# Optimization experiments

Hardware: AMD Instinct MI355X
Metric: run time of the kernel (lower is better)

## Reference

```python
import jax
import jax.numpy as jnp
from jax import lax
import numpy as np

B, C, Hsp, Wsp = 16, 256, 64, 64
E, HID = 4, 128          # num_experts, expert_hidden
RH = 128                 # router_hidden
TOP_K = 1
EPS = 1e-9


def setup_inputs() -> dict:
    key = jax.random.key(0)
    ks = jax.random.split(key, 8)
    s = lambda *shape: 1.0 / np.sqrt(shape[-1])
    x = jax.random.normal(ks[0], (B, C, Hsp, Wsp), dtype=jnp.float32)
    # router: Linear(C->RH), Linear(RH->E)
    Wr1 = jax.random.normal(ks[1], (RH, C), dtype=jnp.float32) * s(RH, C)
    br1 = jnp.zeros((RH,), dtype=jnp.float32)
    Wr2 = jax.random.normal(ks[2], (E, RH), dtype=jnp.float32) * s(E, RH)
    br2 = jnp.zeros((E,), dtype=jnp.float32)
    # experts (stacked over E): 1x1 C->HID, 3x3 HID->HID, 1x1 HID->C, all bias-free
    W1 = jax.random.normal(ks[3], (E, HID, C), dtype=jnp.float32) * s(E, HID, C)
    W2 = jax.random.normal(ks[4], (E, HID, HID, 3, 3), dtype=jnp.float32) * (1.0 / np.sqrt(HID * 9))
    W3 = jax.random.normal(ks[5], (E, C, HID), dtype=jnp.float32) * s(E, C, HID)
    return {"x": x, "Wr1": Wr1, "br1": br1, "Wr2": Wr2, "br2": br2,
            "W1": W1, "W2": W2, "W3": W3}


def reference(x, Wr1, br1, Wr2, br2, W1, W2, W3):
    b = x.shape[0]
    # --- router on globally pooled features ---
    pooled = x.mean(axis=(2, 3))                      # [B, C]
    h = jax.nn.relu(pooled @ Wr1.T + br1)             # [B, RH]
    logits = h @ Wr2.T + br2                          # [B, E]
    probs = jax.nn.softmax(logits, axis=1)
    # top-k masking + renormalize (top_k < num_experts)
    vals, idx = lax.top_k(probs, TOP_K)               # [B, k]
    mask = jnp.zeros_like(probs).at[jnp.arange(b)[:, None], idx].set(vals)
    probs = mask / (mask.sum(axis=1, keepdims=True) + EPS)
    # --- run all experts (as in original) ---
    # 1x1 conv C->HID, per expert:  [B, E, HID, H, W]
    y1 = jax.nn.relu(jnp.einsum('bcij,ehc->behij', x, W1))
    # 3x3 grouped conv (one group per expert), HID->HID
    y1m = y1.reshape(b, E * HID, Hsp, Wsp)
    y2 = lax.conv_general_dilated(
        y1m, W2.reshape(E * HID, HID, 3, 3),
        window_strides=(1, 1), padding='SAME',
        feature_group_count=E,
        dimension_numbers=('NCHW', 'OIHW', 'NCHW'))
    y2 = jax.nn.relu(y2).reshape(b, E, HID, Hsp, Wsp)
    # 1x1 conv HID->C fused with routed weighted sum over experts + residual
    out = jnp.einsum('begij,ecg,be->bcij', y2, W3, probs) + x
    return out
```

## Files before the change

### kernel.cpp

```cpp
#include <hip/hip_runtime.h>

typedef unsigned short ushort_t;
typedef unsigned int uint32;
typedef __attribute__((ext_vector_type(8))) short s16x8;
typedef __attribute__((ext_vector_type(4))) float f32x4;

#define BB   16
#define CC   256
#define NPX  4096
#define EE   4
#define HID  128
#define RHH  128
#define PW   66
#define PPX  (66*66)

__device__ __forceinline__ ushort_t f2bf(float f) {
  uint32 x = __float_as_uint(f);
  x += 0x7fffu + ((x >> 16) & 1u);
  return (ushort_t)(x >> 16);
}
__device__ __forceinline__ void g2l16(const void* g, void* l) {
  __builtin_amdgcn_global_load_lds((const __attribute__((address_space(1))) uint32*)g,
                                   (__attribute__((address_space(3))) uint32*)l, 16, 0, 0);
}

__global__ __launch_bounds__(256)
void k_prep(const float* __restrict__ x, float* __restrict__ pooled,
            const float* __restrict__ W1f, const float* __restrict__ W3f,
            const float* __restrict__ W2f, ushort_t* __restrict__ W1b,
            ushort_t* __restrict__ W3b, ushort_t* __restrict__ W2r,
            ushort_t* __restrict__ y1Tp) {
  int bid = blockIdx.x, t = threadIdx.x;
  if (bid < 4096) {
    int c = bid & 255, b = bid >> 8;
    const float* xg = x + ((size_t)b * CC + c) * NPX;
    float s = 0.f;
#pragma unroll
    for (int k = 0; k < 4; ++k) {
      float4 v = *(const float4*)(xg + (size_t)(k * 256 + t) * 4);
      s += v.x + v.y + v.z + v.w;
    }
#pragma unroll
    for (int o = 32; o >= 1; o >>= 1) s += __shfl_down(s, o, 64);
    __shared__ float wsum[4];
    if ((t & 63) == 0) wsum[t >> 6] = s;
    __syncthreads();
    if (t == 0) pooled[(size_t)b * CC + c] = wsum[0] + wsum[1] + wsum[2] + wsum[3];
  } else if (bid < 4352) {
    int i4 = ((bid - 4096) * 256 + t) * 4;
    const float* src; ushort_t* dst; int off;
    if (i4 < EE * HID * CC) { src = W1f; dst = W1b; off = i4; }
    else { src = W3f; dst = W3b; off = i4 - EE * HID * CC; }
    float4 v = *(const float4*)(src + off);
    ushort4 o;
    o.x = f2bf(v.x); o.y = f2bf(v.y); o.z = f2bf(v.z); o.w = f2bf(v.w);
    *(ushort4*)(dst + off) = o;
  } else if (bid < 4480) {
    int idx = (bid - 4352) * 256 + t;
    int e = idx >> 13;
    int o = (idx >> 6) & 127;
    int ip = (idx & 63) * 2;
    const float* s0 = W2f + ((size_t)((e * 128 + o) * 128) + ip) * 9;
    float v0[9], v1[9];
#pragma unroll
    for (int tp = 0; tp < 9; ++tp) { v0[tp] = s0[tp]; v1[tp] = s0[9 + tp]; }
#pragma unroll
    for (int tp = 0; tp < 9; ++tp) {
      uint32 w = (uint32)f2bf(v0[tp]) | ((uint32)f2bf(v1[tp]) << 16);
      *(uint32*)&W2r[(((size_t)(e * 9 + tp) * 128 + o) * 128) + ip] = w;
    }
  } else {
    int p = (bid - 4480) * 8 + (t >> 5);
    int b = p / 260, i = p % 260;
    int row, col;
    if (i < 66)       { row = 0;       col = i; }
    else if (i < 132) { row = 65;      col = i - 66; }
    else if (i < 196) { row = i - 131; col = 0; }
    else              { row = i - 195; col = 65; }
    uint2* dst = (uint2*)(y1Tp + (((size_t)b * PPX + row * PW + col) * HID) + (t & 31) * 4);
    *dst = make_uint2(0u, 0u);
  }
}

__global__ __launch_bounds__(128)
void k_router(const float* __restrict__ pooled, const float* __restrict__ Wr1,
              const float* __restrict__ br1, const float* __restrict__ Wr2,
              const float* __restrict__ br2, int* __restrict__ eidx,
              float* __restrict__ gatew) {
  int b = blockIdx.x, t = threadIdx.x;
  __shared__ float spool[CC];
  __shared__ float hb[RHH];
  __shared__ float lg[EE];
  for (int cc = t; cc < CC; cc += 128) spool[cc] = pooled[(size_t)b * CC + cc];
  __syncthreads();
  float s0 = 0.f;
  const float* wr = Wr1 + t * CC;
  for (int c = 0; c < CC; ++c) s0 += spool[c] * wr[c];
  float a = br1[t] + s0 * (1.0f / NPX);
  hb[t] = a > 0.f ? a : 0.f;
  __syncthreads();
  if (t < EE) {
    float s = br2[t];
    const float* w2 = Wr2 + t * RHH;
    for (int r = 0; r < RHH; ++r) s += hb[r] * w2[r];
    lg[t] = s;
  }
  __syncthreads();
  if (t == 0) {
    float m = lg[0]; int mi = 0;
    for (int e = 1; e < EE; ++e) if (lg[e] > m) { m = lg[e]; mi = e; }
    float den = 0.f;
    for (int e = 0; e < EE; ++e) den += expf(lg[e] - m);
    float v = 1.0f / den;
    eidx[b] = mi;
    gatew[b] = v / (v + 1e-9f);
  }
}

#define STAGE64B(dstB, srcB_expr)                                         \
  {                                                                       \
    _Pragma("unroll")                                                     \
    for (int s_ = 0; s_ < 4; ++s_) {                                      \
      int ch_ = wave * 4 + s_;                                            \
      int r = ch_ * 8 + (lane >> 3);                                      \
      int kc = ((lane & 7) ^ (lane >> 3)) * 8;                            \
      g2l16(srcB_expr, &dstB[ch_ * 512]);                                 \
    }                                                                     \
  }

#define STAGEW(dst, wsrc, k0v)                                            \
  {                                                                       \
    _Pragma("unroll")                                                     \
    for (int s_ = 0; s_ < 4; ++s_) {                                      \
      int ch_ = wave * 4 + s_;                                            \
      int r_ = ch_ * 8 + (lane >> 3);                                     \
      int kc_ = ((lane & 7) ^ (lane >> 3)) * 8;                           \
      g2l16(wsrc + (size_t)r_ * HID + (k0v) + kc_, &dst[ch_ * 512]);      \
    }                                                                     \
  }

#define MFMA64(At_, Bt_, ACC_)                                            \
  _Pragma("unroll")                                                       \
  for (int kh = 0; kh < 2; ++kh) {                                        \
    s16x8 af[4], bfr[4];                                                  \
    int cidx = ((kh * 4 + (lane >> 4)) ^ (lane & 7)) * 8;                 \
    _Pragma("unroll")                                                     \
    for (int i = 0; i < 4; ++i)                                           \
      af[i] = *(const s16x8*)&At_[(wm + i * 16 + (lane & 15)) * 64 + cidx]; \
    _Pragma("unroll")                                                     \
    for (int j = 0; j < 4; ++j)                                           \
      bfr[j] = *(const s16x8*)&Bt_[(wn + j * 16 + (lane & 15)) * 64 + cidx]; \
    _Pragma("unroll")                                                     \
    for (int i = 0; i < 4; ++i)                                           \
      _Pragma("unroll")                                                   \
      for (int j = 0; j < 4; ++j)                                         \
        ACC_[i][j] = __builtin_amdgcn_mfma_f32_16x16x32_bf16(af[i], bfr[j], ACC_[i][j], 0, 0, 0); \
  }

#define MFMA64H(Hs_, dyv, dxv, Bt_, ACC_)                                 \
  {                                                                       \
    int hbase = ((wm >> 6) + 1 + (dyv)) * 66 + (lane & 15) + 1 + (dxv);   \
    _Pragma("unroll")                                                     \
    for (int kh = 0; kh < 2; ++kh) {                                      \
      s16x8 af[4], bfr[4];                                                \
      int clog = kh * 4 + (lane >> 4);                                    \
      int aoff = (clog ^ (hbase & 7)) << 3;                               \
      int cidx = (clog ^ (lane & 7)) << 3;                                \
      _Pragma("unroll")                                                   \
      for (int i = 0; i < 4; ++i)                                         \
        af[i] = *(const s16x8*)&Hs_[(hbase + i * 16) * 64 + aoff];        \
      _Pragma("unroll")                                                   \
      for (int j = 0; j < 4; ++j)                                         \
        bfr[j] = *(const s16x8*)&Bt_[(wn + j * 16 + (lane & 15)) * 64 + cidx]; \
      _Pragma("unroll")                                                   \
      for (int i = 0; i < 4; ++i)                                         \
        _Pragma("unroll")                                                 \
        for (int j = 0; j < 4; ++j)                                       \
          ACC_[i][j] = __builtin_amdgcn_mfma_f32_16x16x32_bf16(af[i], bfr[j], ACC_[i][j], 0, 0, 0); \
    }                                                                     \
  }

__global__ __launch_bounds__(256)
void k_conv1(const float* __restrict__ x, const ushort_t* __restrict__ W1b,
             const int* __restrict__ eidx, ushort_t* __restrict__ y1Tp) {
  int mt = blockIdx.x, b = blockIdx.y;
  int e = eidx[b];
  int t = threadIdx.x, wave = t >> 6, lane = t & 63;
  int wm = (wave & 1) * 64, wn = (wave >> 1) * 64;
  __shared__ ushort_t smem[128 * 128];
  ushort_t* At = smem;
  ushort_t* Bt = smem + 128 * 64;
  f32x4 acc[4][4] = {};
  const float* xg = x + (size_t)b * CC * NPX + mt * 128;
  const ushort_t* w1 = W1b + (size_t)e * HID * CC;

  int cp = t >> 3;
  int kk = cp * 2;
  int pxb = (t & 7) * 4;

  for (int ks = 0; ks < 4; ++ks) {
    int k0 = ks * 64;
    __syncthreads();
    STAGE64B(Bt, w1 + (size_t)r * CC + k0 + kc);
    {
      const float* r0 = xg + (size_t)(k0 + kk) * NPX;
      const float* r1 = r0 + NPX;
#pragma unroll
      for (int i = 0; i < 4; ++i) {
        int p = pxb + i * 32;
        float4 va = *(const float4*)(r0 + p);
        float4 vb = *(const float4*)(r1 + p);
#pragma unroll
        for (int q = 0; q < 4; ++q) {
          int m = p + q;
          uint32 v = (uint32)f2bf(((const float*)&va)[q]) |
                     ((uint32)f2bf(((const float*)&vb)[q]) << 16);
          int us = m * 64 + (((kk >> 3) ^ (m & 7)) << 3) + (kk & 7);
          *(uint32*)&At[us] = v;
        }
      }
    }
    __syncthreads();
    MFMA64(At, Bt, acc);
  }
  __syncthreads();
#pragma unroll
  for (int i = 0; i < 4; ++i)
#pragma unroll
    for (int j = 0; j < 4; ++j)
#pragma unroll
      for (int r = 0; r < 4; ++r) {
        int m = wm + i * 16 + (lane >> 4) * 4 + r;
        int n = wn + j * 16 + (lane & 15);
        float v = acc[i][j][r];
        smem[m * 128 + (((n >> 3) ^ (m & 7)) << 3) + (n & 7)] = f2bf(v > 0.f ? v : 0.f);
      }
  __syncthreads();
  ushort_t* yb = y1Tp + (size_t)b * PPX * HID;
#pragma unroll
  for (int it = 0; it < 8; ++it) {
    int idx = it * 256 + t;
    int row = idx >> 4, ch = idx & 15;
    int prow = mt * 2 + (row >> 6) + 1, pcol = (row & 63) + 1;
    uint4 v = *(const uint4*)&smem[row * 128 + ((ch ^ (row & 7)) << 3)];
    *(uint4*)(yb + ((size_t)prow * PW + pcol) * HID + ch * 8) = v;
  }
}

__global__ __launch_bounds__(256, 2)
void k_conv23(const ushort_t* __restrict__ y1Tp, const ushort_t* __restrict__ W2r,
              const ushort_t* __restrict__ W3b, const float* __restrict__ x,
              const int* __restrict__ eidx, const float* __restrict__ gatew,
              float* __restrict__ out) {
  int mt = blockIdx.x, b = blockIdx.y;
  int e = eidx[b];
  float gw = gatew[b];
  int t = threadIdx.x, wave = t >> 6, lane = t & 63;
  int wm = (wave & 1) * 64, wn = (wave >> 1) * 64;
  __shared__ ushort_t Hs[4 * 66 * 64];
  __shared__ ushort_t Wb0[128 * 64];
  __shared__ ushort_t Wb1[128 * 64];
  const ushort_t* yb = y1Tp + (size_t)b * PPX * HID;
  const ushort_t* w2e = W2r + (size_t)e * 9 * HID * HID;
  asm volatile("" :: "v"(gw), "s"(e));

  f32x4 acc[4][4] = {};
  for (int ks = 0; ks < 2; ++ks) {
    int k0 = ks * 64;
    __syncthreads();
#pragma unroll
    for (int it = 0; it < 9; ++it) {
      if (it < 8 || wave == 0) {
        int q = it * 256 + t;
        int p = q >> 3, slot = q & 7;
        g2l16(yb + ((size_t)(mt * 132 + p)) * HID + k0 + ((slot ^ (p & 7)) << 3),
              &Hs[(it * 256 + wave * 64) * 8]);
      }
    }
    STAGEW(Wb0, w2e + 0 * HID * HID, k0);
    __syncthreads();
#pragma unroll
    for (int tap = 0; tap < 9; ++tap) {
      ushort_t* cur = (tap & 1) ? Wb1 : Wb0;
      ushort_t* nxt = (tap & 1) ? Wb0 : Wb1;
      if (tap < 8) {
        STAGEW(nxt, w2e + (tap + 1) * HID * HID, k0);
        asm volatile("s_waitcnt vmcnt(4)" ::: "memory");
      } else {
        asm volatile("s_waitcnt vmcnt(0)" ::: "memory");
      }
      __builtin_amdgcn_s_barrier();
      MFMA64H(Hs, tap / 3 - 1, tap % 3 - 1, cur, acc);
      __builtin_amdgcn_s_barrier();
    }
  }
  ushort_t (*y2s)[128 * 64] = (ushort_t (*)[128 * 64])Hs;
#pragma unroll
  for (int i = 0; i < 4; ++i)
#pragma unroll
    for (int j = 0; j < 4; ++j)
#pragma unroll
      for (int r = 0; r < 4; ++r) {
        int m = wm + i * 16 + (lane >> 4) * 4 + r;
        int n = wn + j * 16 + (lane & 15);
        float v = acc[i][j][r];
        ushort_t bv = f2bf(v > 0.f ? v : 0.f);
        int nn = n & 63;
        ushort_t* buf = (n < 64) ? y2s[0] : y2s[1];
        buf[m * 64 + ((nn >> 3) ^ (m & 7)) * 8 + (nn & 7)] = bv;
      }
  f32x4 acc3[2][4][4] = {};
  const ushort_t* w3 = W3b + (size_t)e * CC * HID;
#pragma unroll
  for (int h = 0; h < 2; ++h) {
#pragma unroll
    for (int ks = 0; ks < 2; ++ks) {
      ushort_t* bt = (ks == 0) ? Wb0 : Wb1;
      STAGEW(bt, w3 + (size_t)h * 128 * HID, ks * 64);
      __syncthreads();
      MFMA64(y2s[ks], bt, acc3[h]);
    }
  }
  float* Tf = (float*)Hs;
  for (int h = 0; h < 2; ++h) {
    for (int jj = 0; jj < 4; ++jj) {
      __syncthreads();
      if ((wn >> 6) == (jj >> 1)) {
        int j0 = (jj & 1) * 2;
#pragma unroll
        for (int jd = 0; jd < 2; ++jd) {
          int cl = jd * 16 + (lane & 15);
#pragma unroll
          for (int i = 0; i < 4; ++i) {
            int pb = wm + i * 16 + (lane >> 4) * 4;
            *(f32x4*)&Tf[cl * 132 + pb] = acc3[h][i][j0 + jd];
          }
        }
      }
      __syncthreads();
#pragma unroll
      for (int it = 0; it < 4; ++it) {
        int idx = it * 256 + t;
        int crow = idx >> 5;
        int p4 = (idx & 31) * 4;
        int c = h * 128 + jj * 32 + crow;
        int px = mt * 128 + p4;
        size_t base = ((size_t)b * CC + c) * NPX + px;
        f32x4 vv = *(const f32x4*)&Tf[crow * 132 + p4];
        f32x4 xa = *(const f32x4*)(x + base);
        vv = gw * vv + xa;
        __builtin_nontemporal_store(vv, (f32x4*)(out + base));
      }
    }
  }
}

extern "C" void kernel_launch(void* const* d_in, const int* in_sizes, int n_in,
                              void* d_out, int out_size, void* d_ws, size_t ws_size,
                              hipStream_t stream) {
  const float* x   = (const float*)d_in[0];
  const float* Wr1 = (const float*)d_in[1];
  const float* br1 = (const float*)d_in[2];
  const float* Wr2 = (const float*)d_in[3];
  const float* br2 = (const float*)d_in[4];
  const float* W1  = (const float*)d_in[5];
  const float* W2  = (const float*)d_in[6];
  const float* W3  = (const float*)d_in[7];
  float* out = (float*)d_out;

  char* ws = (char*)d_ws;
  int*      eidx   = (int*)ws;
  float*    gatew  = (float*)(ws + 64);
  float*    pooled = (float*)(ws + 256);
  ushort_t* W1b    = (ushort_t*)(ws + 16640);
  ushort_t* W3b    = (ushort_t*)(ws + 278784);
  ushort_t* W2r    = (ushort_t*)(ws + 540928);
  ushort_t* y1Tp   = (ushort_t*)(ws + 1720576);

  k_prep  <<<5000, 256, 0, stream>>>(x, pooled, W1, W3, W2, W1b, W3b, W2r, y1Tp);
  k_router<<<16, 128, 0, stream>>>(pooled, Wr1, br1, Wr2, br2, eidx, gatew);
  k_conv1 <<<dim3(32, 16), 256, 0, stream>>>(x, W1b, eidx, y1Tp);
  k_conv23<<<dim3(32, 16), 256, 0, stream>>>(y1Tp, W2r, W3b, x, eidx, gatew, out);
}
```

Baseline: 184.7 us.

## Inline router into conv kernels and pipeline weight/halo/residual loads

Removes the separate router kernel launch. Each conv block now recomputes the router inline from the pooled features, using a transposed Wr1 that k_prep writes for coalesced reads. In k_conv23 the 3x3 tap loop is software-pipelined across both K halves and into the W3 stage, and the second halo load moves to after the first half. W3 staging is double-buffered, and x residual loads are prefetched one step ahead of the epilogue stores. MFMA sections get raised wave priority. This trades redundant per-block router work and more barriers for one fewer launch and better load/compute overlap.

```diff
diff --git a/kernel.cpp b/kernel.cpp
--- a/kernel.cpp
+++ b/kernel.cpp
@@ -24,11 +24,16 @@
                                    (__attribute__((address_space(3))) uint32*)l, 16, 0, 0);
 }
 
+#define LGKM0  asm volatile("s_waitcnt lgkmcnt(0)" ::: "memory")
+#define SBAR   __builtin_amdgcn_s_barrier()
+#define SCHED0 __builtin_amdgcn_sched_barrier(0)
+
 __global__ __launch_bounds__(256)
 void k_prep(const float* __restrict__ x, float* __restrict__ pooled,
             const float* __restrict__ W1f, const float* __restrict__ W3f,
-            const float* __restrict__ W2f, ushort_t* __restrict__ W1b,
-            ushort_t* __restrict__ W3b, ushort_t* __restrict__ W2r,
+            const float* __restrict__ W2f, const float* __restrict__ Wr1,
+            ushort_t* __restrict__ W1b, ushort_t* __restrict__ W3b,
+            ushort_t* __restrict__ W2r, float* __restrict__ Wr1T,
             ushort_t* __restrict__ y1Tp) {
   int bid = blockIdx.x, t = threadIdx.x;
   if (bid < 4096) {
@@ -69,8 +74,16 @@
       uint32 w = (uint32)f2bf(v0[tp]) | ((uint32)f2bf(v1[tp]) << 16);
       *(uint32*)&W2r[(((size_t)(e * 9 + tp) * 128 + o) * 128) + ip] = w;
     }
+  } else if (bid < 4512) {
+    int i4 = ((bid - 4480) * 256 + t) * 4;
+    int rh = i4 >> 8, c = i4 & 255;
+    float4 v = *(const float4*)(Wr1 + i4);
+    Wr1T[(size_t)(c + 0) * RHH + rh] = v.x;
+    Wr1T[(size_t)(c + 1) * RHH + rh] = v.y;
+    Wr1T[(size_t)(c + 2) * RHH + rh] = v.z;
+    Wr1T[(size_t)(c + 3) * RHH + rh] = v.w;
   } else {
-    int p = (bid - 4480) * 8 + (t >> 5);
+    int p = (bid - 4512) * 8 + (t >> 5);
     int b = p / 260, i = p % 260;
     int row, col;
     if (i < 66)       { row = 0;       col = i; }
@@ -79,41 +92,6 @@
     else              { row = i - 195; col = 65; }
     uint2* dst = (uint2*)(y1Tp + (((size_t)b * PPX + row * PW + col) * HID) + (t & 31) * 4);
     *dst = make_uint2(0u, 0u);
-  }
-}
-
-__global__ __launch_bounds__(128)
-void k_router(const float* __restrict__ pooled, const float* __restrict__ Wr1,
-              const float* __restrict__ br1, const float* __restrict__ Wr2,
-              const float* __restrict__ br2, int* __restrict__ eidx,
-              float* __restrict__ gatew) {
-  int b = blockIdx.x, t = threadIdx.x;
-  __shared__ float spool[CC];
-  __shared__ float hb[RHH];
-  __shared__ float lg[EE];
-  for (int cc = t; cc < CC; cc += 128) spool[cc] = pooled[(size_t)b * CC + cc];
-  __syncthreads();
-  float s0 = 0.f;
-  const float* wr = Wr1 + t * CC;
-  for (int c = 0; c < CC; ++c) s0 += spool[c] * wr[c];
-  float a = br1[t] + s0 * (1.0f / NPX);
-  hb[t] = a > 0.f ? a : 0.f;
-  __syncthreads();
-  if (t < EE) {
-    float s = br2[t];
-    const float* w2 = Wr2 + t * RHH;
-    for (int r = 0; r < RHH; ++r) s += hb[r] * w2[r];
-    lg[t] = s;
-  }
-  __syncthreads();
-  if (t == 0) {
-    float m = lg[0]; int mi = 0;
-    for (int e = 1; e < EE; ++e) if (lg[e] > m) { m = lg[e]; mi = e; }
-    float den = 0.f;
-    for (int e = 0; e < EE; ++e) den += expf(lg[e] - m);
-    float v = 1.0f / den;
-    eidx[b] = mi;
-    gatew[b] = v / (v + 1e-9f);
   }
 }
 
@@ -180,16 +158,57 @@
     }                                                                     \
   }
 
+__device__ __forceinline__ void router_inline(
+    const float* __restrict__ pooled, const float* __restrict__ Wr1T,
+    const float* __restrict__ br1, const float* __restrict__ Wr2,
+    const float* __restrict__ br2, float* scratch, int b, int t,
+    int* e_out, float* gw_out) {
+  float* spool = scratch;
+  float* hbp   = spool + 256;
+  float* lgp   = hbp + 128;
+  float* gwp   = lgp + 4;
+  int*   eip   = (int*)(gwp + 1);
+  if (t < 64) ((float4*)spool)[t] = ((const float4*)(pooled + (size_t)b * CC))[t];
+  LGKM0; SBAR; SCHED0;
+  if (t < RHH) {
+    float aa = 0.f;
+    for (int c = 0; c < CC; ++c) aa += spool[c] * Wr1T[(size_t)c * RHH + t];
+    float av = br1[t] + aa * (1.0f / NPX);
+    hbp[t] = av > 0.f ? av : 0.f;
+  }
+  LGKM0; SBAR; SCHED0;
+  if (t < EE) {
+    float sv = br2[t];
+    const float* w2 = Wr2 + t * RHH;
+    for (int r = 0; r < RHH; ++r) sv += hbp[r] * w2[r];
+    lgp[t] = sv;
+  }
+  LGKM0; SBAR; SCHED0;
+  if (t == 0) {
+    float m = lgp[0]; int mi = 0;
+    for (int ee = 1; ee < EE; ++ee) if (lgp[ee] > m) { m = lgp[ee]; mi = ee; }
+    float den = 0.f;
+    for (int ee = 0; ee < EE; ++ee) den += expf(lgp[ee] - m);
+    float v = 1.0f / den;
+    *eip = mi; *gwp = v / (v + 1e-9f);
+  }
+  LGKM0; SBAR; SCHED0;
+  *e_out = *eip; *gw_out = *gwp;
+}
+
 __global__ __launch_bounds__(256)
 void k_conv1(const float* __restrict__ x, const ushort_t* __restrict__ W1b,
-             const int* __restrict__ eidx, ushort_t* __restrict__ y1Tp) {
+             const float* __restrict__ pooled, const float* __restrict__ Wr1T,
+             const float* __restrict__ br1, const float* __restrict__ Wr2,
+             const float* __restrict__ br2, ushort_t* __restrict__ y1Tp) {
   int mt = blockIdx.x, b = blockIdx.y;
-  int e = eidx[b];
   int t = threadIdx.x, wave = t >> 6, lane = t & 63;
   int wm = (wave & 1) * 64, wn = (wave >> 1) * 64;
   __shared__ ushort_t smem[128 * 128];
   ushort_t* At = smem;
   ushort_t* Bt = smem + 128 * 64;
+  int e; float gw;
+  router_inline(pooled, Wr1T, br1, Wr2, br2, (float*)smem, b, t, &e, &gw);
   f32x4 acc[4][4] = {};
   const float* xg = x + (size_t)b * CC * NPX + mt * 128;
   const ushort_t* w1 = W1b + (size_t)e * HID * CC;
@@ -250,24 +269,18 @@
 __global__ __launch_bounds__(256, 2)
 void k_conv23(const ushort_t* __restrict__ y1Tp, const ushort_t* __restrict__ W2r,
               const ushort_t* __restrict__ W3b, const float* __restrict__ x,
-              const int* __restrict__ eidx, const float* __restrict__ gatew,
-              float* __restrict__ out) {
+              const float* __restrict__ pooled, const float* __restrict__ Wr1T,
+              const float* __restrict__ br1, const float* __restrict__ Wr2,
+              const float* __restrict__ br2, float* __restrict__ out) {
   int mt = blockIdx.x, b = blockIdx.y;
-  int e = eidx[b];
-  float gw = gatew[b];
   int t = threadIdx.x, wave = t >> 6, lane = t & 63;
   int wm = (wave & 1) * 64, wn = (wave >> 1) * 64;
   __shared__ ushort_t Hs[4 * 66 * 64];
   __shared__ ushort_t Wb0[128 * 64];
   __shared__ ushort_t Wb1[128 * 64];
   const ushort_t* yb = y1Tp + (size_t)b * PPX * HID;
-  const ushort_t* w2e = W2r + (size_t)e * 9 * HID * HID;
-  asm volatile("" :: "v"(gw), "s"(e));
-
-  f32x4 acc[4][4] = {};
-  for (int ks = 0; ks < 2; ++ks) {
-    int k0 = ks * 64;
-    __syncthreads();
+
+  auto halo_stage = [&](int k0) {
 #pragma unroll
     for (int it = 0; it < 9; ++it) {
       if (it < 8 || wave == 0) {
@@ -277,22 +290,35 @@
               &Hs[(it * 256 + wave * 64) * 8]);
       }
     }
-    STAGEW(Wb0, w2e + 0 * HID * HID, k0);
-    __syncthreads();
+  };
+
+  halo_stage(0);
+  int e; float gw;
+  router_inline(pooled, Wr1T, br1, Wr2, br2, (float*)Wb1, b, t, &e, &gw);
+  const ushort_t* w2e = W2r + (size_t)e * 9 * HID * HID;
+  const ushort_t* w3  = W3b + (size_t)e * CC * HID;
+  STAGEW(Wb0, w2e, 0);
+  __syncthreads();
+
+  f32x4 acc[4][4] = {};
+#pragma unroll
+  for (int ks = 0; ks < 2; ++ks) {
 #pragma unroll
     for (int tap = 0; tap < 9; ++tap) {
-      ushort_t* cur = (tap & 1) ? Wb1 : Wb0;
-      ushort_t* nxt = (tap & 1) ? Wb0 : Wb1;
-      if (tap < 8) {
-        STAGEW(nxt, w2e + (tap + 1) * HID * HID, k0);
-        asm volatile("s_waitcnt vmcnt(4)" ::: "memory");
-      } else {
-        asm volatile("s_waitcnt vmcnt(0)" ::: "memory");
-      }
-      __builtin_amdgcn_s_barrier();
+      int par = (tap + ks * 9) & 1;
+      ushort_t* cur = par ? Wb1 : Wb0;
+      ushort_t* nxt = par ? Wb0 : Wb1;
+      if (tap < 8)       { STAGEW(nxt, w2e + (size_t)(tap + 1) * HID * HID, ks * 64); }
+      else if (ks == 0)  { STAGEW(nxt, w2e, 64); }
+      else               { STAGEW(nxt, w3, 0); }
+      asm volatile("s_waitcnt vmcnt(4)" ::: "memory");
+      SBAR; SCHED0;
+      __builtin_amdgcn_s_setprio(1);
       MFMA64H(Hs, tap / 3 - 1, tap % 3 - 1, cur, acc);
-      __builtin_amdgcn_s_barrier();
-    }
+      __builtin_amdgcn_s_setprio(0);
+      SBAR;
+    }
+    if (ks == 0) halo_stage(64);
   }
   ushort_t (*y2s)[128 * 64] = (ushort_t (*)[128 * 64])Hs;
 #pragma unroll
@@ -310,48 +336,68 @@
         buf[m * 64 + ((nn >> 3) ^ (m & 7)) * 8 + (nn & 7)] = bv;
       }
   f32x4 acc3[2][4][4] = {};
-  const ushort_t* w3 = W3b + (size_t)e * CC * HID;
-#pragma unroll
-  for (int h = 0; h < 2; ++h) {
-#pragma unroll
-    for (int ks = 0; ks < 2; ++ks) {
-      ushort_t* bt = (ks == 0) ? Wb0 : Wb1;
-      STAGEW(bt, w3 + (size_t)h * 128 * HID, ks * 64);
-      __syncthreads();
-      MFMA64(y2s[ks], bt, acc3[h]);
-    }
+#pragma unroll
+  for (int s = 0; s < 4; ++s) {
+    ushort_t* cur = (s & 1) ? Wb1 : Wb0;
+    ushort_t* nxt = (s & 1) ? Wb0 : Wb1;
+    if (s < 3) {
+      int s1 = s + 1;
+      STAGEW(nxt, w3 + (size_t)((s1 >> 1) * 128) * HID, (s1 & 1) * 64);
+      asm volatile("s_waitcnt vmcnt(4)" ::: "memory");
+    } else {
+      asm volatile("s_waitcnt vmcnt(0)" ::: "memory");
+    }
+    if (s == 0) LGKM0;
+    SBAR; SCHED0;
+    __builtin_amdgcn_s_setprio(1);
+    MFMA64(y2s[s & 1], cur, acc3[s >> 1]);
+    __builtin_amdgcn_s_setprio(0);
+    SBAR;
   }
   float* Tf = (float*)Hs;
-  for (int h = 0; h < 2; ++h) {
-    for (int jj = 0; jj < 4; ++jj) {
-      __syncthreads();
-      if ((wn >> 6) == (jj >> 1)) {
-        int j0 = (jj & 1) * 2;
-#pragma unroll
-        for (int jd = 0; jd < 2; ++jd) {
-          int cl = jd * 16 + (lane & 15);
-#pragma unroll
-          for (int i = 0; i < 4; ++i) {
-            int pb = wm + i * 16 + (lane >> 4) * 4;
-            *(f32x4*)&Tf[cl * 132 + pb] = acc3[h][i][j0 + jd];
-          }
+  const float* xb = x + (size_t)b * CC * NPX + mt * 128;
+  f32x4 xpre[4];
+#pragma unroll
+  for (int it = 0; it < 4; ++it) {
+    int idx = it * 256 + t, crow = idx >> 5, p4 = (idx & 31) * 4;
+    xpre[it] = *(const f32x4*)(xb + (size_t)crow * NPX + p4);
+  }
+#pragma unroll
+  for (int s = 0; s < 8; ++s) {
+    int h = s >> 2, jj = s & 3;
+    if ((wn >> 6) == (jj >> 1)) {
+      int j0 = (jj & 1) * 2;
+#pragma unroll
+      for (int jd = 0; jd < 2; ++jd) {
+        int cl = jd * 16 + (lane & 15);
+#pragma unroll
+        for (int i = 0; i < 4; ++i) {
+          int pb = wm + i * 16 + (lane >> 4) * 4;
+          *(f32x4*)&Tf[cl * 132 + pb] = acc3[h][i][j0 + jd];
         }
       }
-      __syncthreads();
+    }
+    LGKM0; SBAR; SCHED0;
+    f32x4 xc[4];
+#pragma unroll
+    for (int it = 0; it < 4; ++it) xc[it] = xpre[it];
+    if (s < 7) {
+      int s1 = s + 1, h1 = s1 >> 2, jj1 = s1 & 3;
 #pragma unroll
       for (int it = 0; it < 4; ++it) {
-        int idx = it * 256 + t;
-        int crow = idx >> 5;
-        int p4 = (idx & 31) * 4;
-        int c = h * 128 + jj * 32 + crow;
-        int px = mt * 128 + p4;
-        size_t base = ((size_t)b * CC + c) * NPX + px;
-        f32x4 vv = *(const f32x4*)&Tf[crow * 132 + p4];
-        f32x4 xa = *(const f32x4*)(x + base);
-        vv = gw * vv + xa;
-        __builtin_nontemporal_store(vv, (f32x4*)(out + base));
-      }
-    }
+        int idx = it * 256 + t, crow = idx >> 5, p4 = (idx & 31) * 4;
+        xpre[it] = *(const f32x4*)(xb + (size_t)(h1 * 128 + jj1 * 32 + crow) * NPX + p4);
+      }
+    }
+#pragma unroll
+    for (int it = 0; it < 4; ++it) {
+      int idx = it * 256 + t, crow = idx >> 5, p4 = (idx & 31) * 4;
+      int c = h * 128 + jj * 32 + crow;
+      f32x4 vv = *(const f32x4*)&Tf[crow * 132 + p4];
+      vv = gw * vv + xc[it];
+      __builtin_nontemporal_store(vv, (f32x4*)(out + ((size_t)b * CC + c) * NPX + mt * 128 + p4));
+    }
+    SBAR;
   }
 }
 
@@ -369,16 +415,14 @@
   float* out = (float*)d_out;
 
   char* ws = (char*)d_ws;
-  int*      eidx   = (int*)ws;
-  float*    gatew  = (float*)(ws + 64);
   float*    pooled = (float*)(ws + 256);
   ushort_t* W1b    = (ushort_t*)(ws + 16640);
   ushort_t* W3b    = (ushort_t*)(ws + 278784);
   ushort_t* W2r    = (ushort_t*)(ws + 540928);
-  ushort_t* y1Tp   = (ushort_t*)(ws + 1720576);
-
-  k_prep  <<<5000, 256, 0, stream>>>(x, pooled, W1, W3, W2, W1b, W3b, W2r, y1Tp);
-  k_router<<<16, 128, 0, stream>>>(pooled, Wr1, br1, Wr2, br2, eidx, gatew);
-  k_conv1 <<<dim3(32, 16), 256, 0, stream>>>(x, W1b, eidx, y1Tp);
-  k_conv23<<<dim3(32, 16), 256, 0, stream>>>(y1Tp, W2r, W3b, x, eidx, gatew, out);
-}
+  float*    Wr1T   = (float*)(ws + 1720576);
+  ushort_t* y1Tp   = (ushort_t*)(ws + 1851648);
+
+  k_prep  <<<5032, 256, 0, stream>>>(x, pooled, W1, W3, W2, Wr1, W1b, W3b, W2r, Wr1T, y1Tp);
+  k_conv1 <<<dim3(32, 16), 256, 0, stream>>>(x, W1b, pooled, Wr1T, br1, Wr2, br2, y1Tp);
+  k_conv23<<<dim3(32, 16), 256, 0, stream>>>(y1Tp, W2r, W3b, x, pooled, Wr1T, br1, Wr2, br2, out);
+}
```

New measurement: 203.6 us. +10.2%, slower.

## Fuse expert 1x1 conv into the 3x3/1x1 conv kernel with halo recompute

Applied to the files above, without the earlier changes.

Removes the separate conv1 kernel and its padded bf16 y1 intermediate in global memory. Each block now computes its own y1 tile, including a one-row halo above and below, directly from x into shared memory, zero-fills the left and right padding columns, and then runs the 3x3 and final 1x1 convs. This saves a kernel launch and the global write and read of y1, and the prep kernel no longer zeroes the padding. In exchange, the halo rows mean each block does about twice the conv1 MFMA work and reads more x, and the per-block dependency chain gets longer.

```diff
diff --git a/kernel.cpp b/kernel.cpp
--- a/kernel.cpp
+++ b/kernel.cpp
@@ -11,8 +11,6 @@
 #define EE   4
 #define HID  128
 #define RHH  128
-#define PW   66
-#define PPX  (66*66)
 
 __device__ __forceinline__ ushort_t f2bf(float f) {
   uint32 x = __float_as_uint(f);
@@ -28,8 +26,7 @@
 void k_prep(const float* __restrict__ x, float* __restrict__ pooled,
             const float* __restrict__ W1f, const float* __restrict__ W3f,
             const float* __restrict__ W2f, ushort_t* __restrict__ W1b,
-            ushort_t* __restrict__ W3b, ushort_t* __restrict__ W2r,
-            ushort_t* __restrict__ y1Tp) {
+            ushort_t* __restrict__ W3b, ushort_t* __restrict__ W2r) {
   int bid = blockIdx.x, t = threadIdx.x;
   if (bid < 4096) {
     int c = bid & 255, b = bid >> 8;
@@ -55,7 +52,7 @@
     ushort4 o;
     o.x = f2bf(v.x); o.y = f2bf(v.y); o.z = f2bf(v.z); o.w = f2bf(v.w);
     *(ushort4*)(dst + off) = o;
-  } else if (bid < 4480) {
+  } else {
     int idx = (bid - 4352) * 256 + t;
     int e = idx >> 13;
     int o = (idx >> 6) & 127;
@@ -69,16 +66,6 @@
       uint32 w = (uint32)f2bf(v0[tp]) | ((uint32)f2bf(v1[tp]) << 16);
       *(uint32*)&W2r[(((size_t)(e * 9 + tp) * 128 + o) * 128) + ip] = w;
     }
-  } else {
-    int p = (bid - 4480) * 8 + (t >> 5);
-    int b = p / 260, i = p % 260;
-    int row, col;
-    if (i < 66)       { row = 0;       col = i; }
-    else if (i < 132) { row = 65;      col = i - 66; }
-    else if (i < 196) { row = i - 131; col = 0; }
-    else              { row = i - 195; col = 65; }
-    uint2* dst = (uint2*)(y1Tp + (((size_t)b * PPX + row * PW + col) * HID) + (t & 31) * 4);
-    *dst = make_uint2(0u, 0u);
   }
 }
 
@@ -117,17 +104,6 @@
   }
 }
 
-#define STAGE64B(dstB, srcB_expr)                                         \
-  {                                                                       \
-    _Pragma("unroll")                                                     \
-    for (int s_ = 0; s_ < 4; ++s_) {                                      \
-      int ch_ = wave * 4 + s_;                                            \
-      int r = ch_ * 8 + (lane >> 3);                                      \
-      int kc = ((lane & 7) ^ (lane >> 3)) * 8;                            \
-      g2l16(srcB_expr, &dstB[ch_ * 512]);                                 \
-    }                                                                     \
-  }
-
 #define STAGEW(dst, wsrc, k0v)                                            \
   {                                                                       \
     _Pragma("unroll")                                                     \
@@ -180,111 +156,109 @@
     }                                                                     \
   }
 
-__global__ __launch_bounds__(256)
-void k_conv1(const float* __restrict__ x, const ushort_t* __restrict__ W1b,
-             const int* __restrict__ eidx, ushort_t* __restrict__ y1Tp) {
-  int mt = blockIdx.x, b = blockIdx.y;
-  int e = eidx[b];
-  int t = threadIdx.x, wave = t >> 6, lane = t & 63;
-  int wm = (wave & 1) * 64, wn = (wave >> 1) * 64;
-  __shared__ ushort_t smem[128 * 128];
-  ushort_t* At = smem;
-  ushort_t* Bt = smem + 128 * 64;
-  f32x4 acc[4][4] = {};
-  const float* xg = x + (size_t)b * CC * NPX + mt * 128;
-  const ushort_t* w1 = W1b + (size_t)e * HID * CC;
-
-  int cp = t >> 3;
-  int kk = cp * 2;
-  int pxb = (t & 7) * 4;
-
-  for (int ks = 0; ks < 4; ++ks) {
-    int k0 = ks * 64;
-    __syncthreads();
-    STAGE64B(Bt, w1 + (size_t)r * CC + k0 + kc);
-    {
-      const float* r0 = xg + (size_t)(k0 + kk) * NPX;
-      const float* r1 = r0 + NPX;
-#pragma unroll
-      for (int i = 0; i < 4; ++i) {
-        int p = pxb + i * 32;
-        float4 va = *(const float4*)(r0 + p);
-        float4 vb = *(const float4*)(r1 + p);
-#pragma unroll
-        for (int q = 0; q < 4; ++q) {
-          int m = p + q;
-          uint32 v = (uint32)f2bf(((const float*)&va)[q]) |
-                     ((uint32)f2bf(((const float*)&vb)[q]) << 16);
-          int us = m * 64 + (((kk >> 3) ^ (m & 7)) << 3) + (kk & 7);
-          *(uint32*)&At[us] = v;
-        }
-      }
-    }
-    __syncthreads();
-    MFMA64(At, Bt, acc);
-  }
-  __syncthreads();
-#pragma unroll
-  for (int i = 0; i < 4; ++i)
-#pragma unroll
-    for (int j = 0; j < 4; ++j)
-#pragma unroll
-      for (int r = 0; r < 4; ++r) {
-        int m = wm + i * 16 + (lane >> 4) * 4 + r;
-        int n = wn + j * 16 + (lane & 15);
-        float v = acc[i][j][r];
-        smem[m * 128 + (((n >> 3) ^ (m & 7)) << 3) + (n & 7)] = f2bf(v > 0.f ? v : 0.f);
-      }
-  __syncthreads();
-  ushort_t* yb = y1Tp + (size_t)b * PPX * HID;
-#pragma unroll
-  for (int it = 0; it < 8; ++it) {
-    int idx = it * 256 + t;
-    int row = idx >> 4, ch = idx & 15;
-    int prow = mt * 2 + (row >> 6) + 1, pcol = (row & 63) + 1;
-    uint4 v = *(const uint4*)&smem[row * 128 + ((ch ^ (row & 7)) << 3)];
-    *(uint4*)(yb + ((size_t)prow * PW + pcol) * HID + ch * 8) = v;
-  }
-}
-
 __global__ __launch_bounds__(256, 2)
-void k_conv23(const ushort_t* __restrict__ y1Tp, const ushort_t* __restrict__ W2r,
-              const ushort_t* __restrict__ W3b, const float* __restrict__ x,
-              const int* __restrict__ eidx, const float* __restrict__ gatew,
-              float* __restrict__ out) {
+void k_fused(const float* __restrict__ x, const ushort_t* __restrict__ W1b,
+             const ushort_t* __restrict__ W2r, const ushort_t* __restrict__ W3b,
+             const int* __restrict__ eidx, const float* __restrict__ gatew,
+             float* __restrict__ out) {
   int mt = blockIdx.x, b = blockIdx.y;
   int e = eidx[b];
   float gw = gatew[b];
   int t = threadIdx.x, wave = t >> 6, lane = t & 63;
   int wm = (wave & 1) * 64, wn = (wave >> 1) * 64;
   __shared__ ushort_t Hs[4 * 66 * 64];
-  __shared__ ushort_t Wb0[128 * 64];
-  __shared__ ushort_t Wb1[128 * 64];
-  const ushort_t* yb = y1Tp + (size_t)b * PPX * HID;
+  __shared__ ushort_t WbA[2 * 128 * 64];
+  ushort_t* Wb0 = WbA;
+  ushort_t* Wb1 = WbA + 128 * 64;
   const ushort_t* w2e = W2r + (size_t)e * 9 * HID * HID;
-  asm volatile("" :: "v"(gw), "s"(e));
+  const float* xg = x + (size_t)b * CC * NPX;
+  int px0 = mt * 128 - 64;
+  int cp = t >> 3, kk = cp * 2, pxb = (t & 7) * 4;
 
   f32x4 acc[4][4] = {};
-  for (int ks = 0; ks < 2; ++ks) {
-    int k0 = ks * 64;
+#pragma unroll 1
+  for (int kh = 0; kh < 2; ++kh) {
+    int k0 = kh * 64;
+    f32x4 acc1[4][4] = {};
+    const ushort_t* w1h = W1b + ((size_t)e * HID + k0) * CC;
+#pragma unroll 1
+    for (int cc = 0; cc < 4; ++cc) {
+      int c0 = cc * 64;
+      __syncthreads();
+      {
+#pragma unroll
+        for (int s_ = 0; s_ < 2; ++s_) {
+          int ch2 = wave * 128 + s_ * 64 + lane;
+          int r_ = ch2 >> 3, slot = ch2 & 7;
+          g2l16(w1h + (size_t)r_ * CC + c0 + ((slot ^ (r_ & 7)) << 3),
+                &Hs[(wave * 128 + s_ * 64) * 8]);
+        }
+      }
+      {
+        const float* r0 = xg + (size_t)(c0 + kk) * NPX + px0;
+        const float* r1 = r0 + NPX;
+#pragma unroll
+        for (int i = 0; i < 8; ++i) {
+          int p = pxb + i * 32;
+          int rp = px0 + p;
+          float4 va, vb;
+          if (rp >= 0 && rp < NPX) { va = *(const float4*)(r0 + p); vb = *(const float4*)(r1 + p); }
+          else { va = make_float4(0.f, 0.f, 0.f, 0.f); vb = va; }
+#pragma unroll
+          for (int q = 0; q < 4; ++q) {
+            int m = p + q;
+            uint32 v = (uint32)f2bf(((const float*)&va)[q]) |
+                       ((uint32)f2bf(((const float*)&vb)[q]) << 16);
+            int us = m * 64 + (((kk >> 3) ^ (m & 7)) << 3) + (kk & 7);
+            *(uint32*)&WbA[us] = v;
+          }
+        }
+      }
+      __syncthreads();
+#pragma unroll
+      for (int khk = 0; khk < 2; ++khk) {
+        s16x8 af[4], bfr[4];
+        int clog = khk * 4 + (lane >> 4);
+        int cidx = (clog ^ (lane & 7)) * 8;
+#pragma unroll
+        for (int i = 0; i < 4; ++i)
+          af[i] = *(const s16x8*)&WbA[(wave * 64 + i * 16 + (lane & 15)) * 64 + cidx];
+#pragma unroll
+        for (int j = 0; j < 4; ++j)
+          bfr[j] = *(const s16x8*)&Hs[(j * 16 + (lane & 15)) * 64 + cidx];
+#pragma unroll
+        for (int i = 0; i < 4; ++i)
+#pragma unroll
+          for (int j = 0; j < 4; ++j)
+            acc1[i][j] = __builtin_amdgcn_mfma_f32_16x16x32_bf16(af[i], bfr[j], acc1[i][j], 0, 0, 0);
+      }
+    }
     __syncthreads();
-#pragma unroll
-    for (int it = 0; it < 9; ++it) {
-      if (it < 8 || wave == 0) {
-        int q = it * 256 + t;
-        int p = q >> 3, slot = q & 7;
-        g2l16(yb + ((size_t)(mt * 132 + p)) * HID + k0 + ((slot ^ (p & 7)) << 3),
-              &Hs[(it * 256 + wave * 64) * 8]);
-      }
-    }
-    STAGEW(Wb0, w2e + 0 * HID * HID, k0);
+    STAGEW(Wb0, w2e, k0);
+#pragma unroll
+    for (int i = 0; i < 4; ++i)
+#pragma unroll
+      for (int j = 0; j < 4; ++j)
+#pragma unroll
+        for (int r = 0; r < 4; ++r) {
+          int m = wave * 64 + i * 16 + (lane >> 4) * 4 + r;
+          int h = j * 16 + (lane & 15);
+          int pix = (m >> 6) * 66 + (m & 63) + 1;
+          float v = acc1[i][j][r];
+          Hs[pix * 64 + (((h >> 3) ^ (pix & 7)) << 3) + (h & 7)] = f2bf(v > 0.f ? v : 0.f);
+        }
+    {
+      int row8 = t >> 5;
+      int pix = (row8 >> 1) * 66 + (row8 & 1) * 65;
+      ((uint32*)&Hs[pix * 64])[t & 31] = 0u;
+    }
     __syncthreads();
 #pragma unroll
     for (int tap = 0; tap < 9; ++tap) {
       ushort_t* cur = (tap & 1) ? Wb1 : Wb0;
       ushort_t* nxt = (tap & 1) ? Wb0 : Wb1;
       if (tap < 8) {
-        STAGEW(nxt, w2e + (tap + 1) * HID * HID, k0);
+        STAGEW(nxt, w2e + (size_t)(tap + 1) * HID * HID, k0);
         asm volatile("s_waitcnt vmcnt(4)" ::: "memory");
       } else {
         asm volatile("s_waitcnt vmcnt(0)" ::: "memory");
@@ -294,6 +268,7 @@
       __builtin_amdgcn_s_barrier();
     }
   }
+  __syncthreads();
   ushort_t (*y2s)[128 * 64] = (ushort_t (*)[128 * 64])Hs;
 #pragma unroll
   for (int i = 0; i < 4; ++i)
@@ -316,7 +291,7 @@
 #pragma unroll
     for (int ks = 0; ks < 2; ++ks) {
       ushort_t* bt = (ks == 0) ? Wb0 : Wb1;
-      STAGEW(bt, w3 + (size_t)h * 128 * HID, ks * 64);
+      STAGEW(bt, w3 + (size_t)(h * 128) * HID, ks * 64);
       __syncthreads();
       MFMA64(y2s[ks], bt, acc3[h]);
     }
@@ -375,10 +350,8 @@
   ushort_t* W1b    = (ushort_t*)(ws + 16640);
   ushort_t* W3b    = (ushort_t*)(ws + 278784);
   ushort_t* W2r    = (ushort_t*)(ws + 540928);
-  ushort_t* y1Tp   = (ushort_t*)(ws + 1720576);
-
-  k_prep  <<<5000, 256, 0, stream>>>(x, pooled, W1, W3, W2, W1b, W3b, W2r, y1Tp);
+
+  k_prep  <<<4480, 256, 0, stream>>>(x, pooled, W1, W3, W2, W1b, W3b, W2r);
   k_router<<<16, 128, 0, stream>>>(pooled, Wr1, br1, Wr2, br2, eidx, gatew);
-  k_conv1 <<<dim3(32, 16), 256, 0, stream>>>(x, W1b, eidx, y1Tp);
-  k_conv23<<<dim3(32, 16), 256, 0, stream>>>(y1Tp, W2r, W3b, x, eidx, gatew, out);
-}
+  k_fused <<<dim3(32, 16), 256, 0, stream>>>(x, W1b, W2r, W3b, eidx, gatew, out);
+}
```

Result: slower. 238.9 us (+29.3%).

## Fuse router into pooling kernel via last-block atomic counter; prefetch x in conv1

Applied to the files above, without the earlier changes.

Removes the separate router kernel launch. Each batch's 256 pooling blocks bump an atomic counter, and the last block to finish computes the router MLP, softmax and top-1 in place. This needs a memset of the counters before each run. Separately, conv1 now register-prefetches the next K-slice of x during the MFMA, hiding global load latency at the cost of more registers. A barrier is also added before the conv3 stage.

```diff
diff --git a/kernel.cpp b/kernel.cpp
--- a/kernel.cpp
+++ b/kernel.cpp
@@ -26,9 +26,14 @@
 
 __global__ __launch_bounds__(256)
 void k_prep(const float* __restrict__ x, float* __restrict__ pooled,
+            int* __restrict__ cnt,
             const float* __restrict__ W1f, const float* __restrict__ W3f,
-            const float* __restrict__ W2f, ushort_t* __restrict__ W1b,
-            ushort_t* __restrict__ W3b, ushort_t* __restrict__ W2r,
+            const float* __restrict__ W2f, const float* __restrict__ Wr1,
+            const float* __restrict__ br1, const float* __restrict__ Wr2,
+            const float* __restrict__ br2,
+            ushort_t* __restrict__ W1b, ushort_t* __restrict__ W3b,
+            ushort_t* __restrict__ W2r,
+            int* __restrict__ eidx, float* __restrict__ gatew,
             ushort_t* __restrict__ y1Tp) {
   int bid = blockIdx.x, t = threadIdx.x;
   if (bid < 4096) {
@@ -43,9 +48,62 @@
 #pragma unroll
     for (int o = 32; o >= 1; o >>= 1) s += __shfl_down(s, o, 64);
     __shared__ float wsum[4];
+    __shared__ int lastf;
     if ((t & 63) == 0) wsum[t >> 6] = s;
     __syncthreads();
-    if (t == 0) pooled[(size_t)b * CC + c] = wsum[0] + wsum[1] + wsum[2] + wsum[3];
+    if (t == 0) {
+      float tot = wsum[0] + wsum[1] + wsum[2] + wsum[3];
+      __hip_atomic_store(&pooled[(size_t)b * CC + c], tot,
+                         __ATOMIC_RELEASE, __HIP_MEMORY_SCOPE_AGENT);
+      int old = __hip_atomic_fetch_add(&cnt[b], 1,
+                                       __ATOMIC_ACQ_REL, __HIP_MEMORY_SCOPE_AGENT);
+      lastf = (old == 255) ? 1 : 0;
+    }
+    __syncthreads();
+    if (lastf) {
+      __shared__ float spool[CC];
+      __shared__ float ha[256];
+      __shared__ float hbuf[RHH];
+      __shared__ float lg2[8];
+      spool[t] = __hip_atomic_load(&pooled[(size_t)b * CC + t],
+                                   __ATOMIC_ACQUIRE, __HIP_MEMORY_SCOPE_AGENT);
+      __syncthreads();
+      {
+        int rh = t & 127, hf = t >> 7;
+        const float* wr = Wr1 + (size_t)rh * CC + hf * 128;
+        const float* sp = spool + hf * 128;
+        float a = 0.f;
+        for (int c2 = 0; c2 < 128; ++c2) a += sp[c2] * wr[c2];
+        ha[hf * 128 + rh] = a;
+      }
+      __syncthreads();
+      if (t < RHH) {
+        float av = br1[t] + (ha[t] + ha[128 + t]) * (1.0f / NPX);
+        hbuf[t] = av > 0.f ? av : 0.f;
+      }
+      __syncthreads();
+      if (t < 8) {
+        int e4 = t & 3, hf = t >> 2;
+        const float* w2 = Wr2 + (size_t)e4 * RHH + hf * 64;
+        const float* hh = hbuf + hf * 64;
+        float sv = 0.f;
+        for (int r = 0; r < 64; ++r) sv += hh[r] * w2[r];
+        lg2[t] = sv;
+      }
+      __syncthreads();
+      if (t == 0) {
+        float lgv[4];
+#pragma unroll
+        for (int ee = 0; ee < 4; ++ee) lgv[ee] = br2[ee] + lg2[ee] + lg2[4 + ee];
+        float m = lgv[0]; int mi = 0;
+        for (int ee = 1; ee < 4; ++ee) if (lgv[ee] > m) { m = lgv[ee]; mi = ee; }
+        float den = 0.f;
+        for (int ee = 0; ee < 4; ++ee) den += expf(lgv[ee] - m);
+        float v = 1.0f / den;
+        eidx[b] = mi;
+        gatew[b] = v / (v + 1e-9f);
+      }
+    }
   } else if (bid < 4352) {
     int i4 = ((bid - 4096) * 256 + t) * 4;
     const float* src; ushort_t* dst; int off;
@@ -79,41 +137,6 @@
     else              { row = i - 195; col = 65; }
     uint2* dst = (uint2*)(y1Tp + (((size_t)b * PPX + row * PW + col) * HID) + (t & 31) * 4);
     *dst = make_uint2(0u, 0u);
-  }
-}
-
-__global__ __launch_bounds__(128)
-void k_router(const float* __restrict__ pooled, const float* __restrict__ Wr1,
-              const float* __restrict__ br1, const float* __restrict__ Wr2,
-              const float* __restrict__ br2, int* __restrict__ eidx,
-              float* __restrict__ gatew) {
-  int b = blockIdx.x, t = threadIdx.x;
-  __shared__ float spool[CC];
-  __shared__ float hb[RHH];
-  __shared__ float lg[EE];
-  for (int cc = t; cc < CC; cc += 128) spool[cc] = pooled[(size_t)b * CC + cc];
-  __syncthreads();
-  float s0 = 0.f;
-  const float* wr = Wr1 + t * CC;
-  for (int c = 0; c < CC; ++c) s0 += spool[c] * wr[c];
-  float a = br1[t] + s0 * (1.0f / NPX);
-  hb[t] = a > 0.f ? a : 0.f;
-  __syncthreads();
-  if (t < EE) {
-    float s = br2[t];
-    const float* w2 = Wr2 + t * RHH;
-    for (int r = 0; r < RHH; ++r) s += hb[r] * w2[r];
-    lg[t] = s;
-  }
-  __syncthreads();
-  if (t == 0) {
-    float m = lg[0]; int mi = 0;
-    for (int e = 1; e < EE; ++e) if (lg[e] > m) { m = lg[e]; mi = e; }
-    float den = 0.f;
-    for (int e = 0; e < EE; ++e) den += expf(lg[e] - m);
-    float v = 1.0f / den;
-    eidx[b] = mi;
-    gatew[b] = v / (v + 1e-9f);
   }
 }
 
@@ -198,29 +221,44 @@
   int kk = cp * 2;
   int pxb = (t & 7) * 4;
 
+  float4 va[4], vb[4];
+  {
+    const float* r0 = xg + (size_t)kk * NPX;
+    const float* r1 = r0 + NPX;
+#pragma unroll
+    for (int i = 0; i < 4; ++i) {
+      va[i] = *(const float4*)(r0 + pxb + i * 32);
+      vb[i] = *(const float4*)(r1 + pxb + i * 32);
+    }
+  }
   for (int ks = 0; ks < 4; ++ks) {
     int k0 = ks * 64;
     __syncthreads();
     STAGE64B(Bt, w1 + (size_t)r * CC + k0 + kc);
     {
-      const float* r0 = xg + (size_t)(k0 + kk) * NPX;
-      const float* r1 = r0 + NPX;
 #pragma unroll
       for (int i = 0; i < 4; ++i) {
         int p = pxb + i * 32;
-        float4 va = *(const float4*)(r0 + p);
-        float4 vb = *(const float4*)(r1 + p);
 #pragma unroll
         for (int q = 0; q < 4; ++q) {
           int m = p + q;
-          uint32 v = (uint32)f2bf(((const float*)&va)[q]) |
-                     ((uint32)f2bf(((const float*)&vb)[q]) << 16);
+          uint32 v = (uint32)f2bf(((const float*)&va[i])[q]) |
+                     ((uint32)f2bf(((const float*)&vb[i])[q]) << 16);
           int us = m * 64 + (((kk >> 3) ^ (m & 7)) << 3) + (kk & 7);
           *(uint32*)&At[us] = v;
         }
       }
     }
     __syncthreads();
+    if (ks < 3) {
+      const float* r0 = xg + (size_t)(k0 + 64 + kk) * NPX;
+      const float* r1 = r0 + NPX;
+#pragma unroll
+      for (int i = 0; i < 4; ++i) {
+        va[i] = *(const float4*)(r0 + pxb + i * 32);
+        vb[i] = *(const float4*)(r1 + pxb + i * 32);
+      }
+    }
     MFMA64(At, Bt, acc);
   }
   __syncthreads();
@@ -277,14 +315,14 @@
               &Hs[(it * 256 + wave * 64) * 8]);
       }
     }
-    STAGEW(Wb0, w2e + 0 * HID * HID, k0);
+    STAGEW(Wb0, w2e, k0);
     __syncthreads();
 #pragma unroll
     for (int tap = 0; tap < 9; ++tap) {
       ushort_t* cur = (tap & 1) ? Wb1 : Wb0;
       ushort_t* nxt = (tap & 1) ? Wb0 : Wb1;
       if (tap < 8) {
-        STAGEW(nxt, w2e + (tap + 1) * HID * HID, k0);
+        STAGEW(nxt, w2e + (size_t)(tap + 1) * HID * HID, k0);
         asm volatile("s_waitcnt vmcnt(4)" ::: "memory");
       } else {
         asm volatile("s_waitcnt vmcnt(0)" ::: "memory");
@@ -309,6 +347,7 @@
         ushort_t* buf = (n < 64) ? y2s[0] : y2s[1];
         buf[m * 64 + ((nn >> 3) ^ (m & 7)) * 8 + (nn & 7)] = bv;
       }
+  __syncthreads();
   f32x4 acc3[2][4][4] = {};
   const ushort_t* w3 = W3b + (size_t)e * CC * HID;
 #pragma unroll
@@ -316,7 +355,7 @@
 #pragma unroll
     for (int ks = 0; ks < 2; ++ks) {
       ushort_t* bt = (ks == 0) ? Wb0 : Wb1;
-      STAGEW(bt, w3 + (size_t)h * 128 * HID, ks * 64);
+      STAGEW(bt, w3 + (size_t)(h * 128) * HID, ks * 64);
       __syncthreads();
       MFMA64(y2s[ks], bt, acc3[h]);
     }
@@ -372,13 +411,15 @@
   int*      eidx   = (int*)ws;
   float*    gatew  = (float*)(ws + 64);
   float*    pooled = (float*)(ws + 256);
-  ushort_t* W1b    = (ushort_t*)(ws + 16640);
-  ushort_t* W3b    = (ushort_t*)(ws + 278784);
-  ushort_t* W2r    = (ushort_t*)(ws + 540928);
-  ushort_t* y1Tp   = (ushort_t*)(ws + 1720576);
-
-  k_prep  <<<5000, 256, 0, stream>>>(x, pooled, W1, W3, W2, W1b, W3b, W2r, y1Tp);
-  k_router<<<16, 128, 0, stream>>>(pooled, Wr1, br1, Wr2, br2, eidx, gatew);
+  int*      cnt    = (int*)(ws + 16640);
+  ushort_t* W1b    = (ushort_t*)(ws + 16896);
+  ushort_t* W3b    = (ushort_t*)(ws + 279040);
+  ushort_t* W2r    = (ushort_t*)(ws + 541184);
+  ushort_t* y1Tp   = (ushort_t*)(ws + 1720832);
+
+  hipMemsetAsync(cnt, 0, 64, stream);
+  k_prep  <<<5000, 256, 0, stream>>>(x, pooled, cnt, W1, W3, W2, Wr1, br1, Wr2, br2,
+                                     W1b, W3b, W2r, eidx, gatew, y1Tp);
   k_conv1 <<<dim3(32, 16), 256, 0, stream>>>(x, W1b, eidx, y1Tp);
   k_conv23<<<dim3(32, 16), 256, 0, stream>>>(y1Tp, W2r, W3b, x, eidx, gatew, out);
 }
```

Result: slower. 429.1 us (+132.2%).
